# Performance work log

Hardware: AMD Instinct MI355X
Metric: run time of the kernel (lower is better)

The kernel has to match this reference:

```python
import jax, jax.numpy as jnp
import numpy as np

D0, D1, D2, D3 = 128, 256, 512, 256
B, L = 64, 1024


def _glorot(key, shape):
    fan_in = shape[0]
    return jax.random.normal(key, shape, dtype=jnp.float32) / np.sqrt(fan_in)


def setup_inputs() -> dict:
    key = jax.random.key(0)
    ks = jax.random.split(key, 16)
    return {
        "hid_r": jax.random.normal(ks[0], (B, L, D3), dtype=jnp.float32),
        "in_mask": jnp.ones((B, L), dtype=jnp.float32),
        "init_in": jnp.zeros((B, 1, D0), dtype=jnp.float32),
        "h0": jnp.zeros((1, B, D2), dtype=jnp.float32),
        "c0": jnp.zeros((1, B, D2), dtype=jnp.float32),
        # lin_1: D0 -> D1 (Linear + ReLU)
        "W1": _glorot(ks[1], (D0, D1)), "b1": jnp.zeros((D1,), jnp.float32),
        # LSTM: input D1, hidden D2, gates order i,f,g,o (PyTorch)
        "Wih": _glorot(ks[2], (D1, 4 * D2)), "Whh": _glorot(ks[3], (D2, 4 * D2)),
        "bih": jnp.zeros((4 * D2,), jnp.float32), "bhh": jnp.zeros((4 * D2,), jnp.float32),
        # lin_2: D2 -> D3
        "W2": _glorot(ks[4], (D2, D3)), "b2": jnp.zeros((D3,), jnp.float32),
        # attention projections q,k,v (D3 -> D3)
        "Wq": _glorot(ks[5], (D3, D3)), "bq": jnp.zeros((D3,), jnp.float32),
        "Wk": _glorot(ks[6], (D3, D3)), "bk": jnp.zeros((D3,), jnp.float32),
        "Wv": _glorot(ks[7], (D3, D3)), "bv": jnp.zeros((D3,), jnp.float32),
        # lin_3: D3 -> D0
        "W3": _glorot(ks[8], (D3, D0)), "b3": jnp.zeros((D0,), jnp.float32),
    }


def reference(hid_r, in_mask, init_in, h0, c0, W1, b1, Wih, Whh, bih, bhh,
              W2, b2, Wq, bq, Wk, bk, Wv, bv, W3, b3):
    length = hid_r.shape[1]
    scale = 1.0 / np.sqrt(D3).astype(np.float32)
    # k/v projections of the (fixed) encoder memory, hoisted out of the loop
    k = hid_r @ Wk + bk            # [B, L, D3]
    v = hid_r @ Wv + bv            # [B, L, D3]
    mask_bias = jnp.where(in_mask == 0, -1e9, 0.0)  # [B, L]

    def step(carry, _):
        h, c, x = carry            # h,c: [B,D2], x: [B,D0]
        a = jax.nn.relu(x @ W1 + b1)                       # lin_1
        gates = a @ Wih + bih + h @ Whh + bhh              # [B, 4*D2]
        i_g, f_g, g_g, o_g = jnp.split(gates, 4, axis=-1)
        c = jax.nn.sigmoid(f_g) * c + jax.nn.sigmoid(i_g) * jnp.tanh(g_g)
        h = jax.nn.sigmoid(o_g) * jnp.tanh(c)
        dx = jax.nn.relu(h @ W2 + b2)                      # lin_2 -> [B,D3]
        q = dx @ Wq + bq                                   # [B, D3]
        scores = jnp.einsum('bd,bld->bl', q, k) * scale + mask_bias
        attn = jax.nn.softmax(scores, axis=-1)             # [B, L]
        ctx = jnp.einsum('bl,bld->bd', attn, v)            # [B, D3]
        y = jax.nn.relu(ctx @ W3 + b3)                     # lin_3 -> [B,D0]
        return (h, c, y), (y, attn)

    carry0 = (h0[0], c0[0], init_in[:, 0, :])
    _, (ys, attns) = jax.lax.scan(step, carry0, None, length=length)
    outputs = jnp.transpose(ys, (1, 0, 2)) * in_mask[:, :, None]  # mask_it
    attention_weights = jnp.transpose(attns, (1, 0, 2))           # [B, L, L]
    return outputs, attention_weights
```

## Files before the change

### kernel.cpp

```cpp
#include <hip/hip_runtime.h>

typedef unsigned short u16;
typedef unsigned int u32;
typedef __attribute__((ext_vector_type(8))) short bf16x8;
typedef __attribute__((ext_vector_type(8))) unsigned short u16x8;
typedef __attribute__((ext_vector_type(4))) unsigned short u16x4;
typedef __attribute__((ext_vector_type(4))) float f32x4;

#define DI static __device__ __forceinline__

constexpr size_t OFF_WKQ  = 0;
constexpr size_t OFF_WVW  = OFF_WKQ  + 256*256*4;
constexpr size_t OFF_WB   = OFF_WVW  + 256*128*4;
constexpr size_t OFF_BYV  = OFF_WB   + 256*4;
constexpr size_t OFF_BG   = OFF_BYV  + 128*4;
constexpr size_t OFF_W2T  = OFF_BG   + 2048*4;
constexpr size_t OFF_W1F  = OFF_W2T  + 256*512*2;
constexpr size_t OFF_WIHF = OFF_W1F  + 16*4*64*8*2;
constexpr size_t OFF_WHHF = OFF_WIHF + 128*8*64*8*2;
constexpr size_t OFF_KT   = OFF_WHHF + 128*16*64*8*2;
constexpr size_t OFF_VW   = OFF_KT   + (size_t)64*1024*256*2;
constexpr size_t OFF_S0   = OFF_VW   + (size_t)64*1024*128*2;
constexpr size_t OFF_CB   = OFF_S0   + 65536*4;
constexpr size_t OFF_HF   = OFF_CB   + 64*512*4;
constexpr size_t OFF_HFR  = OFF_HF   + 64*512*4;
constexpr size_t OFF_SC   = OFF_HFR  + 2*16*4*64*8*2;
constexpr size_t OFF_PART = OFF_SC   + 2*64*1024*4;

DI float bf2f(u16 u){ unsigned int v = ((unsigned int)u) << 16; return __uint_as_float(v); }
DI u16 f2bf(float f){ unsigned int u = __float_as_uint(f); unsigned int r = (u + 0x7FFFu + ((u>>16)&1u)) >> 16; return (u16)r; }
DI float sigm(float x){ return 1.f/(1.f + __expf(-x)); }
DI float tanh_(float x){ return 1.f - 2.f/(__expf(2.f*x) + 1.f); }

DI int fragIdx(int m, int k){ return (((k>>5)*4 + (m>>4))*64 + ((m&15) | (((k>>3)&3)<<4)))*8 + (k&7); }

__global__ __launch_bounds__(256) void kPrep(char* ws,
    const float* W1, const float* Wih, const float* Whh, const float* W2,
    const float* Wq, const float* bq, const float* Wk, const float* bk,
    const float* Wv, const float* bv, const float* W3, const float* b3,
    const float* bih, const float* bhh, const float* c0, const float* h0)
{
  const int wg = blockIdx.x, tid = threadIdx.x;
  if (wg < 64) {
    float* Wkq = (float*)(ws + OFF_WKQ);
    for (int rr = 0; rr < 4; ++rr) {
      const int e = wg*4 + rr;
      float acc = 0.f;
      for (int d = 0; d < 256; ++d) acc = fmaf(Wk[e*256+d], Wq[tid*256+d], acc);
      Wkq[e*256 + tid] = acc * 0.0625f;
    }
  } else if (wg < 96) {
    float* Wvw = (float*)(ws + OFF_WVW);
    if (tid < 128) {
      for (int rr = 0; rr < 8; ++rr) {
        const int e = (wg-64)*8 + rr;
        float acc = 0.f;
        for (int d = 0; d < 256; ++d) acc = fmaf(Wv[e*256+d], W3[d*128+tid], acc);
        Wvw[e*128 + tid] = acc;
      }
    }
  } else if (wg == 96) {
    float* wb = (float*)(ws + OFF_WB);
    float acc = 0.f;
    for (int d = 0; d < 256; ++d) acc = fmaf(Wk[tid*256+d], bq[d], acc);
    wb[tid] = acc * 0.0625f;
    if (tid < 128) {
      float* byv = (float*)(ws + OFF_BYV);
      float a2 = b3[tid];
      for (int d = 0; d < 256; ++d) a2 = fmaf(bv[d], W3[d*128+tid], a2);
      byv[tid] = a2;
    }
  } else if (wg == 97) {
    float* bg = (float*)(ws + OFF_BG);
    for (int j = tid; j < 2048; j += 256) bg[j] = bih[j] + bhh[j];
  } else if (wg < 106) {
    u16* W2T = (u16*)(ws + OFF_W2T);
    const int n0 = (wg - 98)*32;
    for (int nn = 0; nn < 32; ++nn) {
      const int n = n0 + nn;
      for (int k = tid; k < 512; k += 256) W2T[n*512 + k] = f2bf(W2[k*256 + n]);
    }
  } else if (wg < 122) {
    u16* W1f = (u16*)(ws + OFF_W1F);
    const int nt2 = wg - 106;
    for (int idx = tid; idx < 4*512; idx += 256) {
      const int kt2 = idx >> 9, rem = idx & 511, lane = rem >> 3, i = rem & 7;
      const int k = kt2*32 + (lane>>4)*8 + i, n = nt2*16 + (lane&15);
      W1f[((nt2*4+kt2)*64+lane)*8+i] = f2bf(W1[k*256+n]);
    }
  } else if (wg < 250) {
    u16* Wihf = (u16*)(ws + OFF_WIHF);
    const int nt = wg - 122;
    for (int idx = tid; idx < 8*512; idx += 256) {
      const int kt = idx >> 9, rem = idx & 511, lane = rem >> 3, i = rem & 7;
      const int k = kt*32 + (lane>>4)*8 + i, r = lane & 15;
      const int gcol = (r>>2)*512 + nt*4 + (r&3);
      Wihf[((nt*8+kt)*64+lane)*8+i] = f2bf(Wih[k*2048 + gcol]);
    }
  } else if (wg < 378) {
    u16* Whhf = (u16*)(ws + OFF_WHHF);
    const int nt = wg - 250;
    for (int idx = tid; idx < 16*512; idx += 256) {
      const int kt = idx >> 9, rem = idx & 511, lane = rem >> 3, i = rem & 7;
      const int k = kt*32 + (lane>>4)*8 + i, r = lane & 15;
      const int gcol = (r>>2)*512 + nt*4 + (r&3);
      Whhf[((nt*16+kt)*64+lane)*8+i] = f2bf(Whh[k*2048 + gcol]);
    }
  } else if (wg < 410) {
    float* cb = (float*)(ws + OFF_CB);
    u16* hfr0 = (u16*)(ws + OFF_HFR);
    const int base = (wg - 378)*1024;
    for (int ii = tid; ii < 1024; ii += 256) {
      const int idx = base + ii, b = idx >> 9, j = idx & 511;
      cb[idx] = c0[idx];
      hfr0[fragIdx(b, j)] = f2bf(h0[idx]);
    }
  }
}

__global__ __launch_bounds__(256) void kKTVW(char* __restrict__ ws, const float* __restrict__ hid_r,
                                             const float* __restrict__ in_mask)
{
  const int wg = blockIdx.x, tid = threadIdx.x;
  __shared__ float lh[256*36];
  const float* Wkq = (const float*)(ws + OFF_WKQ);
  const float* Wvw = (const float*)(ws + OFF_WVW);
  const float* wb  = (const float*)(ws + OFF_WB);
  u16* kt = (u16*)(ws + OFF_KT);
  u16* vw = (u16*)(ws + OFF_VW);
  float* s0 = (float*)(ws + OFF_S0);
  const size_t r0 = (size_t)wg * 32;
  for (int idx = tid; idx < 32*256; idx += 256) {
    const int e = idx & 255, r = idx >> 8;
    lh[e*36 + r] = hid_r[(r0 + r)*256 + e];
  }
  __syncthreads();
  float acc[32];
  #pragma unroll
  for (int r = 0; r < 32; ++r) acc[r] = 0.f;
  for (int e = 0; e < 256; ++e) {
    const float wv = Wkq[e*256 + tid];
    #pragma unroll
    for (int r4 = 0; r4 < 8; ++r4) {
      const float4 l4 = *(const float4*)&lh[e*36 + r4*4];
      acc[r4*4+0] = fmaf(l4.x, wv, acc[r4*4+0]);
      acc[r4*4+1] = fmaf(l4.y, wv, acc[r4*4+1]);
      acc[r4*4+2] = fmaf(l4.z, wv, acc[r4*4+2]);
      acc[r4*4+3] = fmaf(l4.w, wv, acc[r4*4+3]);
    }
  }
  for (int r = 0; r < 32; ++r) kt[(r0 + r)*256 + tid] = f2bf(acc[r]);
  if (tid < 128) {
    #pragma unroll
    for (int r = 0; r < 32; ++r) acc[r] = 0.f;
    for (int e = 0; e < 256; ++e) {
      const float wv = Wvw[e*128 + tid];
      #pragma unroll
      for (int r4 = 0; r4 < 8; ++r4) {
        const float4 l4 = *(const float4*)&lh[e*36 + r4*4];
        acc[r4*4+0] = fmaf(l4.x, wv, acc[r4*4+0]);
        acc[r4*4+1] = fmaf(l4.y, wv, acc[r4*4+1]);
        acc[r4*4+2] = fmaf(l4.z, wv, acc[r4*4+2]);
        acc[r4*4+3] = fmaf(l4.w, wv, acc[r4*4+3]);
      }
    }
    for (int r = 0; r < 32; ++r) vw[(r0 + r)*128 + tid] = f2bf(acc[r]);
  } else if (tid < 160) {
    const int r = tid - 128;
    float a3 = 0.f;
    for (int e = 0; e < 256; ++e) a3 = fmaf(lh[e*36 + r], wb[e], a3);
    s0[r0 + r] = a3 + (in_mask[r0 + r] == 0.f ? -1e9f : 0.f);
  }
}

__global__ __launch_bounds__(1024) void kA(char* __restrict__ ws, const float* __restrict__ init_in,
                                           const float* __restrict__ in_mask, const float* __restrict__ b1,
                                           float* __restrict__ dout, int s)
{
  const int wg = blockIdx.x, tid = threadIdx.x;
  const float* part = (const float*)(ws + OFF_PART) + (size_t)((s+1)&1)*(64*8*130);
  const float* byv = (const float*)(ws + OFF_BYV);

  if (wg >= 64) {
    if (s == 0) return;
    const int b = wg - 64, t = s - 1;
    const float* scp = (const float*)(ws + OFF_SC) + (size_t)((s+1)&1)*(64*1024);
    float pm[8], pS[8], m = -1e30f;
    #pragma unroll
    for (int c = 0; c < 8; ++c) { pm[c] = part[(b*8+c)*130]; pS[c] = part[(b*8+c)*130+1]; m = fmaxf(m, pm[c]); }
    float Sv = 0.f;
    #pragma unroll
    for (int c = 0; c < 8; ++c) Sv += pS[c] * __expf(pm[c]-m);
    const float inv = 1.f / Sv;
    float* attn = dout + (size_t)64*1024*128;
    __builtin_nontemporal_store(__expf(scp[b*1024 + tid] - m) * inv,
                                &attn[((size_t)b*1024 + t)*1024 + tid]);
    if (tid < 128) {
      float a2 = 0.f;
      #pragma unroll
      for (int c = 0; c < 8; ++c) a2 += __expf(pm[c]-m) * part[(b*8+c)*130+2+tid];
      const float y = fmaxf(a2*inv + byv[tid], 0.f);
      __builtin_nontemporal_store(y * in_mask[b*1024 + t],
                                  &dout[((size_t)b*1024 + t)*128 + tid]);
    }
    return;
  }

  __shared__ union {
    u16 yfrag[16*64*8];
    struct { float gmerge[8*64*4]; float gtile[64*32]; } s3;
  } shmU;
  __shared__ union {
    u16 afrag[32*64*8];
    float lfac[64*8];
  } shmV;

  if (s == 0) {
    for (int idx = tid; idx < 64*128; idx += 1024) {
      const int b = idx >> 7, d0 = idx & 127;
      shmU.yfrag[fragIdx(b, d0)] = f2bf(init_in[b*128 + d0]);
    }
  } else {
    if (tid < 64) {
      const int b = tid;
      float pm[8], m = -1e30f;
      #pragma unroll
      for (int c = 0; c < 8; ++c) { pm[c] = part[(b*8+c)*130]; m = fmaxf(m, pm[c]); }
      float Sv = 0.f, pf[8];
      #pragma unroll
      for (int c = 0; c < 8; ++c) { pf[c] = __expf(pm[c]-m); Sv += part[(b*8+c)*130+1]*pf[c]; }
      const float inv = 1.f/Sv;
      #pragma unroll
      for (int c = 0; c < 8; ++c) shmV.lfac[b*8+c] = pf[c]*inv;
    }
    __syncthreads();
    for (int idx = tid; idx < 64*128; idx += 1024) {
      const int b = idx >> 7, d0 = idx & 127;
      float a2 = byv[d0];
      #pragma unroll
      for (int c = 0; c < 8; ++c) a2 += shmV.lfac[b*8+c]*part[(b*8+c)*130+2+d0];
      shmU.yfrag[fragIdx(b, d0)] = f2bf(fmaxf(a2, 0.f));
    }
  }
  __syncthreads();
  const int w = tid >> 6, lane = tid & 63;
  {
    const u16* W1f = (const u16*)(ws + OFF_W1F);
    const int mt = w & 3, nb0 = w >> 2;
    for (int k = 0; k < 4; ++k) {
      const int nt2 = nb0 + k*4;
      f32x4 acc = {0.f,0.f,0.f,0.f};
      #pragma unroll
      for (int kt2 = 0; kt2 < 4; ++kt2) {
        bf16x8 av = *(const bf16x8*)&shmU.yfrag[((kt2*4+mt)*64+lane)*8];
        bf16x8 bv = *(const bf16x8*)&W1f[((nt2*4+kt2)*64+lane)*8];
        acc = __builtin_amdgcn_mfma_f32_16x16x32_bf16(av, bv, acc, 0, 0, 0);
      }
      const int col = nt2*16 + (lane&15);
      const float bb = b1[col];
      #pragma unroll
      for (int i = 0; i < 4; ++i) {
        const int b = mt*16 + (lane>>4)*4 + i;
        shmV.afrag[fragIdx(b, col)] = f2bf(fmaxf(acc[i] + bb, 0.f));
      }
    }
  }
  __syncthreads();
  {
    const u16* Wihf = (const u16*)(ws + OFF_WIHF);
    const u16* Whhf = (const u16*)(ws + OFF_WHHF);
    const u16* hfr = (const u16*)(ws + OFF_HFR) + (size_t)(s & 1)*(16*4*64*8);
    const int mt = w & 3, ntile = (w>>2) & 1, khalf = w >> 3;
    const int nt = wg*2 + ntile;
    f32x4 acc = {0.f,0.f,0.f,0.f};
    if (khalf == 0) {
      for (int kt = 0; kt < 8; ++kt) {
        bf16x8 av = *(const bf16x8*)&shmV.afrag[((kt*4+mt)*64+lane)*8];
        bf16x8 bv = *(const bf16x8*)&Wihf[((nt*8+kt)*64+lane)*8];
        acc = __builtin_amdgcn_mfma_f32_16x16x32_bf16(av, bv, acc, 0, 0, 0);
      }
      for (int kt = 0; kt < 4; ++kt) {
        bf16x8 av = *(const bf16x8*)&hfr[((kt*4+mt)*64+lane)*8];
        bf16x8 bv = *(const bf16x8*)&Whhf[((nt*16+kt)*64+lane)*8];
        acc = __builtin_amdgcn_mfma_f32_16x16x32_bf16(av, bv, acc, 0, 0, 0);
      }
    } else {
      for (int kt = 4; kt < 16; ++kt) {
        bf16x8 av = *(const bf16x8*)&hfr[((kt*4+mt)*64+lane)*8];
        bf16x8 bv = *(const bf16x8*)&Whhf[((nt*16+kt)*64+lane)*8];
        acc = __builtin_amdgcn_mfma_f32_16x16x32_bf16(av, bv, acc, 0, 0, 0);
      }
      #pragma unroll
      for (int i = 0; i < 4; ++i) shmU.s3.gmerge[((ntile*4+mt)*64+lane)*4+i] = acc[i];
    }
    __syncthreads();
    if (khalf == 0) {
      const float* bg = (const float*)(ws + OFF_BG);
      const int r = lane & 15;
      const float bb = bg[(r>>2)*512 + nt*4 + (r&3)];
      #pragma unroll
      for (int i = 0; i < 4; ++i) {
        const int b = mt*16 + (lane>>4)*4 + i;
        shmU.s3.gtile[b*32 + ntile*16 + r] = acc[i] + shmU.s3.gmerge[((ntile*4+mt)*64+lane)*4+i] + bb;
      }
    }
  }
  __syncthreads();
  if (tid < 256) {
    const int b = tid >> 2, jj2 = tid & 3;
    float* cb = (float*)(ws + OFF_CB);
    float* hf = (float*)(ws + OFF_HF);
    u16* hfw = (u16*)(ws + OFF_HFR) + (size_t)((s & 1) ^ 1)*(16*4*64*8);
    float hv[2];
    #pragma unroll
    for (int t2 = 0; t2 < 2; ++t2) {
      const int jj = jj2*2 + t2;
      const int j = wg*8 + jj;
      const int cb32 = b*32 + (jj>>2)*16 + (jj&3);
      const float ig = shmU.s3.gtile[cb32 + 0];
      const float fg = shmU.s3.gtile[cb32 + 4];
      const float gg = shmU.s3.gtile[cb32 + 8];
      const float og = shmU.s3.gtile[cb32 + 12];
      const float cold = cb[b*512 + j];
      const float cnew = sigm(fg)*cold + sigm(ig)*tanh_(gg);
      hv[t2] = sigm(og)*tanh_(cnew);
      cb[b*512 + j] = cnew;
    }
    const int j0 = wg*8 + jj2*2;
    *(float2*)&hf[b*512 + j0] = make_float2(hv[0], hv[1]);
    const u32 pw = (u32)f2bf(hv[0]) | ((u32)f2bf(hv[1]) << 16);
    *(u32*)&hfw[fragIdx(b, j0)] = pw;
  }
}

__global__ __launch_bounds__(512, 4) void kB(char* __restrict__ ws, const float* __restrict__ b2, int s)
{
  const int wg = blockIdx.x, tid = threadIdx.x;
  const int b = wg >> 3, ch = wg & 7;
  const int hl = tid & 31, unit = tid >> 5;
  __shared__ union { float red[256*33]; float mrg[16*132]; } U;
  __shared__ float dxl[256];

  const u16* kt = (const u16*)(ws + OFF_KT);
  const u16* vw = (const u16*)(ws + OFF_VW);
  const float* s0 = (const float*)(ws + OFF_S0);
  float* partc = (float*)(ws + OFF_PART) + (size_t)(s&1)*(64*8*130);
  float* scc   = (float*)(ws + OFF_SC)   + (size_t)(s&1)*(64*1024);

  u16x8 kvr[8]; u16x4 vvr[8]; float s0r[8];
  #pragma unroll
  for (int i = 0; i < 8; ++i) {
    const int l = ch*128 + i*16 + unit;
    const size_t row = (size_t)b*1024 + l;
    kvr[i] = *(const u16x8*)(kt + row*256 + hl*8);
    vvr[i] = *(const u16x4*)(vw + row*128 + hl*4);
    s0r[i] = s0[row];
  }

  {
    const float* hb = (const float*)(ws + OFF_HF) + b*512;
    const u16* W2T = (const u16*)(ws + OFF_W2T);
    float hreg[16];
    #pragma unroll
    for (int i = 0; i < 4; ++i) {
      const float4 h4 = *(const float4*)(hb + hl*16 + i*4);
      hreg[i*4+0] = h4.x; hreg[i*4+1] = h4.y; hreg[i*4+2] = h4.z; hreg[i*4+3] = h4.w;
    }
    #pragma unroll
    for (int j = 0; j < 16; ++j) {
      const int n = unit*16 + j;
      const u16x8 w0 = *(const u16x8*)(W2T + n*512 + hl*16);
      const u16x8 w1 = *(const u16x8*)(W2T + n*512 + hl*16 + 8);
      float acc = 0.f;
      #pragma unroll
      for (int i2 = 0; i2 < 8; ++i2) acc = fmaf(hreg[i2], bf2f(w0[i2]), acc);
      #pragma unroll
      for (int i2 = 0; i2 < 8; ++i2) acc = fmaf(hreg[8+i2], bf2f(w1[i2]), acc);
      U.red[n*33 + hl] = acc;
    }
  }
  __syncthreads();
  if (tid < 256) {
    float acc = 0.f;
    #pragma unroll
    for (int l = 0; l < 32; ++l) acc += U.red[tid*33 + l];
    dxl[tid] = fmaxf(acc + b2[tid], 0.f);
  }
  __syncthreads();

  float dxv[8];
  {
    const float4 d0 = *(const float4*)&dxl[hl*8];
    const float4 d1 = *(const float4*)&dxl[hl*8+4];
    dxv[0]=d0.x; dxv[1]=d0.y; dxv[2]=d0.z; dxv[3]=d0.w;
    dxv[4]=d1.x; dxv[5]=d1.y; dxv[6]=d1.z; dxv[7]=d1.w;
  }
  float sums[8];
  #pragma unroll
  for (int i = 0; i < 8; ++i) {
    float sum = 0.f;
    #pragma unroll
    for (int j2 = 0; j2 < 8; ++j2) sum = fmaf(bf2f(kvr[i][j2]), dxv[j2], sum);
    #pragma unroll
    for (int d = 1; d < 32; d <<= 1) sum += __shfl_xor(sum, d, 64);
    sums[i] = sum + s0r[i];
  }
  float keep = 0.f;
  #pragma unroll
  for (int i = 0; i < 8; ++i) if (hl == i) keep = sums[i];
  float m = sums[0];
  #pragma unroll
  for (int i = 1; i < 8; ++i) m = fmaxf(m, sums[i]);
  float S = 0.f, cx0 = 0.f, cx1 = 0.f, cx2 = 0.f, cx3 = 0.f;
  #pragma unroll
  for (int i = 0; i < 8; ++i) {
    const float e2 = __expf(sums[i] - m);
    S += e2;
    cx0 = fmaf(e2, bf2f(vvr[i][0]), cx0);
    cx1 = fmaf(e2, bf2f(vvr[i][1]), cx1);
    cx2 = fmaf(e2, bf2f(vvr[i][2]), cx2);
    cx3 = fmaf(e2, bf2f(vvr[i][3]), cx3);
  }
  if (hl < 8) scc[b*1024 + ch*128 + hl*16 + unit] = keep;
  U.mrg[unit*132 + 4 + hl*4 + 0] = cx0;
  U.mrg[unit*132 + 4 + hl*4 + 1] = cx1;
  U.mrg[unit*132 + 4 + hl*4 + 2] = cx2;
  U.mrg[unit*132 + 4 + hl*4 + 3] = cx3;
  if (hl == 0) { U.mrg[unit*132] = m; U.mrg[unit*132+1] = S; }
  __syncthreads();
  if (tid < 128) {
    float mg = -1e30f;
    for (int u = 0; u < 16; ++u) mg = fmaxf(mg, U.mrg[u*132]);
    float Sg = 0.f, cx = 0.f;
    for (int u = 0; u < 16; ++u) {
      const float f = __expf(U.mrg[u*132] - mg);
      Sg = fmaf(U.mrg[u*132+1], f, Sg);
      cx = fmaf(f, U.mrg[u*132 + 4 + tid], cx);
    }
    partc[(b*8+ch)*130 + 2 + tid] = cx;
    if (tid == 0) { partc[(b*8+ch)*130] = mg; partc[(b*8+ch)*130+1] = Sg; }
  }
}

__global__ __launch_bounds__(1024) void kWLast(char* __restrict__ ws, const float* __restrict__ in_mask,
                                               float* __restrict__ dout)
{
  const int b = blockIdx.x, tid = threadIdx.x;
  const float* part = (const float*)(ws + OFF_PART) + (size_t)(1023&1)*(64*8*130);
  const float* sc   = (const float*)(ws + OFF_SC)   + (size_t)(1023&1)*(64*1024);
  float pm[8], pS[8], m = -1e30f;
  #pragma unroll
  for (int c = 0; c < 8; ++c) { pm[c] = part[(b*8+c)*130]; pS[c] = part[(b*8+c)*130+1]; m = fmaxf(m, pm[c]); }
  float Sv = 0.f;
  #pragma unroll
  for (int c = 0; c < 8; ++c) Sv += pS[c] * __expf(pm[c]-m);
  const float inv = 1.f / Sv;
  float* attn = dout + (size_t)64*1024*128;
  __builtin_nontemporal_store(__expf(sc[b*1024 + tid] - m) * inv,
                              &attn[((size_t)b*1024 + 1023)*1024 + tid]);
  if (tid < 128) {
    const float* byv = (const float*)(ws + OFF_BYV);
    float a2 = 0.f;
    #pragma unroll
    for (int c = 0; c < 8; ++c) a2 += __expf(pm[c]-m) * part[(b*8+c)*130+2+tid];
    const float y = fmaxf(a2*inv + byv[tid], 0.f);
    __builtin_nontemporal_store(y * in_mask[b*1024 + 1023],
                                &dout[((size_t)b*1024 + 1023)*128 + tid]);
  }
}

extern "C" void kernel_launch(void* const* d_in, const int* in_sizes, int n_in,
                              void* d_out, int out_size, void* d_ws, size_t ws_size,
                              hipStream_t stream)
{
  (void)in_sizes; (void)n_in; (void)out_size; (void)ws_size;
  const float* hid_r  = (const float*)d_in[0];
  const float* in_mask= (const float*)d_in[1];
  const float* init_in= (const float*)d_in[2];
  const float* h0     = (const float*)d_in[3];
  const float* c0     = (const float*)d_in[4];
  const float* W1     = (const float*)d_in[5];
  const float* b1     = (const float*)d_in[6];
  const float* Wih    = (const float*)d_in[7];
  const float* Whh    = (const float*)d_in[8];
  const float* bih    = (const float*)d_in[9];
  const float* bhh    = (const float*)d_in[10];
  const float* W2     = (const float*)d_in[11];
  const float* b2     = (const float*)d_in[12];
  const float* Wq     = (const float*)d_in[13];
  const float* bq     = (const float*)d_in[14];
  const float* Wk     = (const float*)d_in[15];
  const float* bk     = (const float*)d_in[16];
  const float* Wv     = (const float*)d_in[17];
  const float* bv     = (const float*)d_in[18];
  const float* W3     = (const float*)d_in[19];
  const float* b3     = (const float*)d_in[20];
  char* ws = (char*)d_ws;
  float* out = (float*)d_out;

  hipLaunchKernelGGL(kPrep, dim3(410), dim3(256), 0, stream, ws,
                     W1, Wih, Whh, W2, Wq, bq, Wk, bk, Wv, bv, W3, b3, bih, bhh, c0, h0);
  hipLaunchKernelGGL(kKTVW, dim3(2048), dim3(256), 0, stream, ws, hid_r, in_mask);
  for (int s = 0; s < 1024; ++s) {
    hipLaunchKernelGGL(kA, dim3(128), dim3(1024), 0, stream, ws, init_in, in_mask, b1, out, s);
    hipLaunchKernelGGL(kB, dim3(512), dim3(512), 0, stream, ws, b2, s);
  }
  hipLaunchKernelGGL(kWLast, dim3(64), dim3(1024), 0, stream, ws, in_mask, out);
}
```

Measured before the change: 29.23 ms.

## Fuse per-step LSTM and attention kernels with in-kernel flag synchronization

Merges the two per-timestep launches into a single kernel of 512 workgroups. Workgroups 0-63 compute the LSTM gates, then spin on global epoch flags until every gate group has published h. Each then computes dx for its batch row and signals the attention workgroups through a per-batch flag. This halves the launch count and the kernel-boundary drains per step, and lets attention work for other batches start without a full grid barrier. The cost is spin-waiting that assumes all workgroups are co-resident, which risks deadlock or contention, plus a redundant dx matvec per batch in the gate workgroups.

```diff
diff --git a/kernel.cpp b/kernel.cpp
--- a/kernel.cpp
+++ b/kernel.cpp
@@ -2,6 +2,7 @@
 
 typedef unsigned short u16;
 typedef unsigned int u32;
+typedef unsigned long long u64;
 typedef __attribute__((ext_vector_type(8))) short bf16x8;
 typedef __attribute__((ext_vector_type(8))) unsigned short u16x8;
 typedef __attribute__((ext_vector_type(4))) unsigned short u16x4;
@@ -26,11 +27,20 @@
 constexpr size_t OFF_HFR  = OFF_HF   + 64*512*4;
 constexpr size_t OFF_SC   = OFF_HFR  + 2*16*4*64*8*2;
 constexpr size_t OFF_PART = OFF_SC   + 2*64*1024*4;
+constexpr size_t OFF_DXG  = OFF_PART + 2*64*8*130*4;
+constexpr size_t OFF_HFL  = OFF_DXG  + 64*256*4;
+constexpr size_t OFF_DXF  = OFF_HFL  + 64*16*4;
 
 DI float bf2f(u16 u){ unsigned int v = ((unsigned int)u) << 16; return __uint_as_float(v); }
 DI u16 f2bf(float f){ unsigned int u = __float_as_uint(f); unsigned int r = (u + 0x7FFFu + ((u>>16)&1u)) >> 16; return (u16)r; }
 DI float sigm(float x){ return 1.f/(1.f + __expf(-x)); }
 DI float tanh_(float x){ return 1.f - 2.f/(__expf(2.f*x) + 1.f); }
+
+DI float aldf(const float* p){ return __hip_atomic_load(p, __ATOMIC_RELAXED, __HIP_MEMORY_SCOPE_AGENT); }
+DI void  astf(float* p, float v){ __hip_atomic_store(p, v, __ATOMIC_RELAXED, __HIP_MEMORY_SCOPE_AGENT); }
+DI void  astu32(u32* p, u32 v){ __hip_atomic_store(p, v, __ATOMIC_RELAXED, __HIP_MEMORY_SCOPE_AGENT); }
+DI u32   aldu32(const u32* p){ return __hip_atomic_load(p, __ATOMIC_RELAXED, __HIP_MEMORY_SCOPE_AGENT); }
+DI void  astu64(u64* p, u64 v){ __hip_atomic_store(p, v, __ATOMIC_RELAXED, __HIP_MEMORY_SCOPE_AGENT); }
 
 DI int fragIdx(int m, int k){ return (((k>>5)*4 + (m>>4))*64 + ((m&15) | (((k>>3)&3)<<4)))*8 + (k&7); }
 
@@ -73,6 +83,8 @@
   } else if (wg == 97) {
     float* bg = (float*)(ws + OFF_BG);
     for (int j = tid; j < 2048; j += 256) bg[j] = bih[j] + bhh[j];
+    u32* fl = (u32*)(ws + OFF_HFL);
+    for (int j = tid; j < 2048; j += 256) fl[j] = 0u;
   } else if (wg < 106) {
     u16* W2T = (u16*)(ws + OFF_W2T);
     const int n0 = (wg - 98)*32;
@@ -173,18 +185,43 @@
   }
 }
 
-__global__ __launch_bounds__(1024) void kA(char* __restrict__ ws, const float* __restrict__ init_in,
-                                           const float* __restrict__ in_mask, const float* __restrict__ b1,
-                                           float* __restrict__ dout, int s)
+struct ShmGates {
+  union {
+    u16 yfrag[16*64*8];
+    float gtile[64*32];
+    struct { float hstage[512]; float dxred[512]; } dxs;
+  } u;
+  union {
+    u16 afrag[32*64*8];
+    float lfac[64*8];
+  } v;
+};
+struct ShmAttn { float mrg[16*132]; float dxl[256]; };
+union Shm { ShmGates g; ShmAttn a; };
+
+__global__ __launch_bounds__(512, 4) void kStep(char* __restrict__ ws, const float* __restrict__ init_in,
+    const float* __restrict__ in_mask, const float* __restrict__ b1, const float* __restrict__ b2,
+    float* __restrict__ dout, int s)
 {
   const int wg = blockIdx.x, tid = threadIdx.x;
+  __shared__ Shm sh;
+
   const float* part = (const float*)(ws + OFF_PART) + (size_t)((s+1)&1)*(64*8*130);
+  float* partc = (float*)(ws + OFF_PART) + (size_t)(s&1)*(64*8*130);
+  const float* scp = (const float*)(ws + OFF_SC) + (size_t)((s+1)&1)*(64*1024);
+  float* scc = (float*)(ws + OFF_SC) + (size_t)(s&1)*(64*1024);
   const float* byv = (const float*)(ws + OFF_BYV);
-
-  if (wg >= 64) {
-    if (s == 0) return;
-    const int b = wg - 64, t = s - 1;
-    const float* scp = (const float*)(ws + OFF_SC) + (size_t)((s+1)&1)*(64*1024);
+  float* HF = (float*)(ws + OFF_HF);
+  float* dxg = (float*)(ws + OFF_DXG);
+  u32* hfl = (u32*)(ws + OFF_HFL);
+  u32* dxf = (u32*)(ws + OFF_DXF);
+  const u32 epoch = (u32)s + 1u;
+
+  int b, ch;
+  if (wg < 64) { b = wg; ch = 7; }
+  else { const int a = wg - 64; b = a / 7; ch = a % 7; }
+
+  if (s > 0 && tid < 256) {
     float pm[8], pS[8], m = -1e30f;
     #pragma unroll
     for (int c = 0; c < 8; ++c) { pm[c] = part[(b*8+c)*130]; pS[c] = part[(b*8+c)*130+1]; m = fmaxf(m, pm[c]); }
@@ -192,253 +229,242 @@
     #pragma unroll
     for (int c = 0; c < 8; ++c) Sv += pS[c] * __expf(pm[c]-m);
     const float inv = 1.f / Sv;
-    float* attn = dout + (size_t)64*1024*128;
-    __builtin_nontemporal_store(__expf(scp[b*1024 + tid] - m) * inv,
-                                &attn[((size_t)b*1024 + t)*1024 + tid]);
+    const int t = s - 1;
     if (tid < 128) {
+      const int l = ch*128 + tid;
+      float* attn = dout + (size_t)64*1024*128;
+      __builtin_nontemporal_store(__expf(scp[b*1024 + l] - m) * inv,
+                                  &attn[((size_t)b*1024 + t)*1024 + l]);
+    } else if (ch == 0) {
+      const int d0 = tid - 128;
       float a2 = 0.f;
       #pragma unroll
-      for (int c = 0; c < 8; ++c) a2 += __expf(pm[c]-m) * part[(b*8+c)*130+2+tid];
-      const float y = fmaxf(a2*inv + byv[tid], 0.f);
+      for (int c = 0; c < 8; ++c) a2 += __expf(pm[c]-m) * part[(b*8+c)*130+2+d0];
+      const float y = fmaxf(a2*inv + byv[d0], 0.f);
       __builtin_nontemporal_store(y * in_mask[b*1024 + t],
-                                  &dout[((size_t)b*1024 + t)*128 + tid]);
-    }
-    return;
-  }
-
-  __shared__ union {
-    u16 yfrag[16*64*8];
-    struct { float gmerge[8*64*4]; float gtile[64*32]; } s3;
-  } shmU;
-  __shared__ union {
-    u16 afrag[32*64*8];
-    float lfac[64*8];
-  } shmV;
-
-  if (s == 0) {
-    for (int idx = tid; idx < 64*128; idx += 1024) {
-      const int b = idx >> 7, d0 = idx & 127;
-      shmU.yfrag[fragIdx(b, d0)] = f2bf(init_in[b*128 + d0]);
-    }
-  } else {
-    if (tid < 64) {
-      const int b = tid;
-      float pm[8], m = -1e30f;
-      #pragma unroll
-      for (int c = 0; c < 8; ++c) { pm[c] = part[(b*8+c)*130]; m = fmaxf(m, pm[c]); }
-      float Sv = 0.f, pf[8];
-      #pragma unroll
-      for (int c = 0; c < 8; ++c) { pf[c] = __expf(pm[c]-m); Sv += part[(b*8+c)*130+1]*pf[c]; }
-      const float inv = 1.f/Sv;
-      #pragma unroll
-      for (int c = 0; c < 8; ++c) shmV.lfac[b*8+c] = pf[c]*inv;
-    }
-    __syncthreads();
-    for (int idx = tid; idx < 64*128; idx += 1024) {
-      const int b = idx >> 7, d0 = idx & 127;
-      float a2 = byv[d0];
-      #pragma unroll
-      for (int c = 0; c < 8; ++c) a2 += shmV.lfac[b*8+c]*part[(b*8+c)*130+2+d0];
-      shmU.yfrag[fragIdx(b, d0)] = f2bf(fmaxf(a2, 0.f));
-    }
-  }
-  __syncthreads();
-  const int w = tid >> 6, lane = tid & 63;
-  {
-    const u16* W1f = (const u16*)(ws + OFF_W1F);
-    const int mt = w & 3, nb0 = w >> 2;
-    for (int k = 0; k < 4; ++k) {
-      const int nt2 = nb0 + k*4;
+                                  &dout[((size_t)b*1024 + t)*128 + d0]);
+    }
+  }
+
+  const int hl = tid & 31, unit = tid >> 5;
+
+  if (wg < 64) {
+    if (s == 0) {
+      for (int idx = tid; idx < 64*128; idx += 512) {
+        const int bb = idx >> 7, d0 = idx & 127;
+        sh.g.u.yfrag[fragIdx(bb, d0)] = f2bf(init_in[bb*128 + d0]);
+      }
+    } else {
+      if (tid < 64) {
+        const int bb = tid;
+        float pm[8], m = -1e30f;
+        #pragma unroll
+        for (int c = 0; c < 8; ++c) { pm[c] = part[(bb*8+c)*130]; m = fmaxf(m, pm[c]); }
+        float Sv = 0.f, pf[8];
+        #pragma unroll
+        for (int c = 0; c < 8; ++c) { pf[c] = __expf(pm[c]-m); Sv += part[(bb*8+c)*130+1]*pf[c]; }
+        const float inv = 1.f/Sv;
+        #pragma unroll
+        for (int c = 0; c < 8; ++c) sh.g.v.lfac[bb*8+c] = pf[c]*inv;
+      }
+      __syncthreads();
+      for (int idx = tid; idx < 64*128; idx += 512) {
+        const int bb = idx >> 7, d0 = idx & 127;
+        float a2 = byv[d0];
+        #pragma unroll
+        for (int c = 0; c < 8; ++c) a2 += sh.g.v.lfac[bb*8+c]*part[(bb*8+c)*130+2+d0];
+        sh.g.u.yfrag[fragIdx(bb, d0)] = f2bf(fmaxf(a2, 0.f));
+      }
+    }
+    __syncthreads();
+    const int w = tid >> 6, lane = tid & 63;
+    {
+      const u16* W1f = (const u16*)(ws + OFF_W1F);
+      const int mt = w & 3, nh = w >> 2;
+      for (int k = 0; k < 8; ++k) {
+        const int nt2 = nh*8 + k;
+        f32x4 acc = {0.f,0.f,0.f,0.f};
+        #pragma unroll
+        for (int kt2 = 0; kt2 < 4; ++kt2) {
+          bf16x8 av = *(const bf16x8*)&sh.g.u.yfrag[((kt2*4+mt)*64+lane)*8];
+          bf16x8 bv = *(const bf16x8*)&W1f[((nt2*4+kt2)*64+lane)*8];
+          acc = __builtin_amdgcn_mfma_f32_16x16x32_bf16(av, bv, acc, 0, 0, 0);
+        }
+        const int col = nt2*16 + (lane&15);
+        const float bb2 = b1[col];
+        #pragma unroll
+        for (int i = 0; i < 4; ++i) {
+          const int bb = mt*16 + (lane>>4)*4 + i;
+          sh.g.v.afrag[fragIdx(bb, col)] = f2bf(fmaxf(acc[i] + bb2, 0.f));
+        }
+      }
+    }
+    __syncthreads();
+    {
+      const u16* Wihf = (const u16*)(ws + OFF_WIHF);
+      const u16* Whhf = (const u16*)(ws + OFF_WHHF);
+      const u16* hfr = (const u16*)(ws + OFF_HFR) + (size_t)(s & 1)*(16*4*64*8);
+      const int mt = w & 3, ntile = w >> 2;
+      const int nt = wg*2 + ntile;
       f32x4 acc = {0.f,0.f,0.f,0.f};
-      #pragma unroll
-      for (int kt2 = 0; kt2 < 4; ++kt2) {
-        bf16x8 av = *(const bf16x8*)&shmU.yfrag[((kt2*4+mt)*64+lane)*8];
-        bf16x8 bv = *(const bf16x8*)&W1f[((nt2*4+kt2)*64+lane)*8];
-        acc = __builtin_amdgcn_mfma_f32_16x16x32_bf16(av, bv, acc, 0, 0, 0);
-      }
-      const int col = nt2*16 + (lane&15);
-      const float bb = b1[col];
-      #pragma unroll
-      for (int i = 0; i < 4; ++i) {
-        const int b = mt*16 + (lane>>4)*4 + i;
-        shmV.afrag[fragIdx(b, col)] = f2bf(fmaxf(acc[i] + bb, 0.f));
-      }
-    }
-  }
-  __syncthreads();
-  {
-    const u16* Wihf = (const u16*)(ws + OFF_WIHF);
-    const u16* Whhf = (const u16*)(ws + OFF_WHHF);
-    const u16* hfr = (const u16*)(ws + OFF_HFR) + (size_t)(s & 1)*(16*4*64*8);
-    const int mt = w & 3, ntile = (w>>2) & 1, khalf = w >> 3;
-    const int nt = wg*2 + ntile;
-    f32x4 acc = {0.f,0.f,0.f,0.f};
-    if (khalf == 0) {
       for (int kt = 0; kt < 8; ++kt) {
-        bf16x8 av = *(const bf16x8*)&shmV.afrag[((kt*4+mt)*64+lane)*8];
+        bf16x8 av = *(const bf16x8*)&sh.g.v.afrag[((kt*4+mt)*64+lane)*8];
         bf16x8 bv = *(const bf16x8*)&Wihf[((nt*8+kt)*64+lane)*8];
         acc = __builtin_amdgcn_mfma_f32_16x16x32_bf16(av, bv, acc, 0, 0, 0);
       }
-      for (int kt = 0; kt < 4; ++kt) {
+      for (int kt = 0; kt < 16; ++kt) {
         bf16x8 av = *(const bf16x8*)&hfr[((kt*4+mt)*64+lane)*8];
         bf16x8 bv = *(const bf16x8*)&Whhf[((nt*16+kt)*64+lane)*8];
         acc = __builtin_amdgcn_mfma_f32_16x16x32_bf16(av, bv, acc, 0, 0, 0);
       }
-    } else {
-      for (int kt = 4; kt < 16; ++kt) {
-        bf16x8 av = *(const bf16x8*)&hfr[((kt*4+mt)*64+lane)*8];
-        bf16x8 bv = *(const bf16x8*)&Whhf[((nt*16+kt)*64+lane)*8];
-        acc = __builtin_amdgcn_mfma_f32_16x16x32_bf16(av, bv, acc, 0, 0, 0);
-      }
-      #pragma unroll
-      for (int i = 0; i < 4; ++i) shmU.s3.gmerge[((ntile*4+mt)*64+lane)*4+i] = acc[i];
-    }
-    __syncthreads();
-    if (khalf == 0) {
+      __syncthreads();
       const float* bg = (const float*)(ws + OFF_BG);
       const int r = lane & 15;
-      const float bb = bg[(r>>2)*512 + nt*4 + (r&3)];
+      const float bb2 = bg[(r>>2)*512 + nt*4 + (r&3)];
       #pragma unroll
       for (int i = 0; i < 4; ++i) {
-        const int b = mt*16 + (lane>>4)*4 + i;
-        shmU.s3.gtile[b*32 + ntile*16 + r] = acc[i] + shmU.s3.gmerge[((ntile*4+mt)*64+lane)*4+i] + bb;
-      }
-    }
-  }
-  __syncthreads();
-  if (tid < 256) {
-    const int b = tid >> 2, jj2 = tid & 3;
-    float* cb = (float*)(ws + OFF_CB);
-    float* hf = (float*)(ws + OFF_HF);
-    u16* hfw = (u16*)(ws + OFF_HFR) + (size_t)((s & 1) ^ 1)*(16*4*64*8);
-    float hv[2];
-    #pragma unroll
-    for (int t2 = 0; t2 < 2; ++t2) {
-      const int jj = jj2*2 + t2;
-      const int j = wg*8 + jj;
-      const int cb32 = b*32 + (jj>>2)*16 + (jj&3);
-      const float ig = shmU.s3.gtile[cb32 + 0];
-      const float fg = shmU.s3.gtile[cb32 + 4];
-      const float gg = shmU.s3.gtile[cb32 + 8];
-      const float og = shmU.s3.gtile[cb32 + 12];
-      const float cold = cb[b*512 + j];
-      const float cnew = sigm(fg)*cold + sigm(ig)*tanh_(gg);
-      hv[t2] = sigm(og)*tanh_(cnew);
-      cb[b*512 + j] = cnew;
-    }
-    const int j0 = wg*8 + jj2*2;
-    *(float2*)&hf[b*512 + j0] = make_float2(hv[0], hv[1]);
-    const u32 pw = (u32)f2bf(hv[0]) | ((u32)f2bf(hv[1]) << 16);
-    *(u32*)&hfw[fragIdx(b, j0)] = pw;
-  }
-}
-
-__global__ __launch_bounds__(512, 4) void kB(char* __restrict__ ws, const float* __restrict__ b2, int s)
-{
-  const int wg = blockIdx.x, tid = threadIdx.x;
-  const int b = wg >> 3, ch = wg & 7;
-  const int hl = tid & 31, unit = tid >> 5;
-  __shared__ union { float red[256*33]; float mrg[16*132]; } U;
-  __shared__ float dxl[256];
-
-  const u16* kt = (const u16*)(ws + OFF_KT);
-  const u16* vw = (const u16*)(ws + OFF_VW);
-  const float* s0 = (const float*)(ws + OFF_S0);
-  float* partc = (float*)(ws + OFF_PART) + (size_t)(s&1)*(64*8*130);
-  float* scc   = (float*)(ws + OFF_SC)   + (size_t)(s&1)*(64*1024);
-
-  u16x8 kvr[8]; u16x4 vvr[8]; float s0r[8];
-  #pragma unroll
-  for (int i = 0; i < 8; ++i) {
-    const int l = ch*128 + i*16 + unit;
-    const size_t row = (size_t)b*1024 + l;
-    kvr[i] = *(const u16x8*)(kt + row*256 + hl*8);
-    vvr[i] = *(const u16x4*)(vw + row*128 + hl*4);
-    s0r[i] = s0[row];
+        const int bb = mt*16 + (lane>>4)*4 + i;
+        sh.g.u.gtile[bb*32 + ntile*16 + r] = acc[i] + bb2;
+      }
+    }
+    __syncthreads();
+    if (tid < 256) {
+      const int bb = tid >> 2, jj2 = tid & 3;
+      float* cb = (float*)(ws + OFF_CB);
+      u16* hfw = (u16*)(ws + OFF_HFR) + (size_t)((s & 1) ^ 1)*(16*4*64*8);
+      float hv[2];
+      #pragma unroll
+      for (int t2 = 0; t2 < 2; ++t2) {
+        const int jj = jj2*2 + t2;
+        const int j = wg*8 + jj;
+        const int cb32 = bb*32 + (jj>>2)*16 + (jj&3);
+        const float ig = sh.g.u.gtile[cb32 + 0];
+        const float fg = sh.g.u.gtile[cb32 + 4];
+        const float gg = sh.g.u.gtile[cb32 + 8];
+        const float og = sh.g.u.gtile[cb32 + 12];
+        const float cold = cb[bb*512 + j];
+        const float cnew = sigm(fg)*cold + sigm(ig)*tanh_(gg);
+        hv[t2] = sigm(og)*tanh_(cnew);
+        cb[bb*512 + j] = cnew;
+      }
+      const int j0 = wg*8 + jj2*2;
+      union { float f[2]; u64 u; } pk; pk.f[0] = hv[0]; pk.f[1] = hv[1];
+      astu64((u64*)&HF[bb*512 + j0], pk.u);
+      const u32 pw = (u32)f2bf(hv[0]) | ((u32)f2bf(hv[1]) << 16);
+      *(u32*)&hfw[fragIdx(bb, j0)] = pw;
+    }
+    __syncthreads();
+    if (tid == 0) astu32(&hfl[wg*16], epoch);
+    if (tid < 64) {
+      for (;;) {
+        const u32 f = aldu32(&hfl[tid*16]);
+        if (__all(f >= epoch)) break;
+        __builtin_amdgcn_s_sleep(1);
+      }
+    }
+    __syncthreads();
+    sh.g.u.dxs.hstage[tid] = aldf(&HF[b*512 + tid]);
+    __syncthreads();
+    float dxval = 0.f;
+    {
+      const u16* W2T = (const u16*)(ws + OFF_W2T);
+      const int n = tid >> 1, kh = tid & 1;
+      float acc = 0.f;
+      for (int kk = 0; kk < 32; ++kk) {
+        const int k = kh*256 + kk*8;
+        const float4 h4a = *(const float4*)&sh.g.u.dxs.hstage[k];
+        const float4 h4b = *(const float4*)&sh.g.u.dxs.hstage[k+4];
+        const u16x8 wv = *(const u16x8*)(W2T + n*512 + k);
+        acc = fmaf(h4a.x, bf2f(wv[0]), acc); acc = fmaf(h4a.y, bf2f(wv[1]), acc);
+        acc = fmaf(h4a.z, bf2f(wv[2]), acc); acc = fmaf(h4a.w, bf2f(wv[3]), acc);
+        acc = fmaf(h4b.x, bf2f(wv[4]), acc); acc = fmaf(h4b.y, bf2f(wv[5]), acc);
+        acc = fmaf(h4b.z, bf2f(wv[6]), acc); acc = fmaf(h4b.w, bf2f(wv[7]), acc);
+      }
+      sh.g.u.dxs.dxred[tid] = acc;
+      __syncthreads();
+      if (tid < 256) dxval = fmaxf(sh.g.u.dxs.dxred[2*tid] + sh.g.u.dxs.dxred[2*tid+1] + b2[tid], 0.f);
+    }
+    __syncthreads();
+    if (tid < 256) {
+      sh.a.dxl[tid] = dxval;
+      astf(&dxg[b*256 + tid], dxval);
+    }
+    __syncthreads();
+    if (tid == 0) astu32(&dxf[b*16], epoch);
+  } else {
+    if (tid == 0) {
+      while (aldu32(&dxf[b*16]) < epoch) __builtin_amdgcn_s_sleep(2);
+    }
+    __syncthreads();
+    if (tid < 256) sh.a.dxl[tid] = aldf(&dxg[b*256 + tid]);
+    __syncthreads();
   }
 
   {
-    const float* hb = (const float*)(ws + OFF_HF) + b*512;
-    const u16* W2T = (const u16*)(ws + OFF_W2T);
-    float hreg[16];
-    #pragma unroll
-    for (int i = 0; i < 4; ++i) {
-      const float4 h4 = *(const float4*)(hb + hl*16 + i*4);
-      hreg[i*4+0] = h4.x; hreg[i*4+1] = h4.y; hreg[i*4+2] = h4.z; hreg[i*4+3] = h4.w;
-    }
-    #pragma unroll
-    for (int j = 0; j < 16; ++j) {
-      const int n = unit*16 + j;
-      const u16x8 w0 = *(const u16x8*)(W2T + n*512 + hl*16);
-      const u16x8 w1 = *(const u16x8*)(W2T + n*512 + hl*16 + 8);
-      float acc = 0.f;
+    const u16* kt = (const u16*)(ws + OFF_KT);
+    const u16* vw = (const u16*)(ws + OFF_VW);
+    const float* s0 = (const float*)(ws + OFF_S0);
+    u16x8 kvr[8]; u16x4 vvr[8]; float s0r[8];
+    #pragma unroll
+    for (int i = 0; i < 8; ++i) {
+      const int l = ch*128 + i*16 + unit;
+      const size_t row = (size_t)b*1024 + l;
+      kvr[i] = *(const u16x8*)(kt + row*256 + hl*8);
+      vvr[i] = *(const u16x4*)(vw + row*128 + hl*4);
+      s0r[i] = s0[row];
+    }
+    float dxv[8];
+    {
+      const float4 d0 = *(const float4*)&sh.a.dxl[hl*8];
+      const float4 d1 = *(const float4*)&sh.a.dxl[hl*8+4];
+      dxv[0]=d0.x; dxv[1]=d0.y; dxv[2]=d0.z; dxv[3]=d0.w;
+      dxv[4]=d1.x; dxv[5]=d1.y; dxv[6]=d1.z; dxv[7]=d1.w;
+    }
+    float sums[8];
+    #pragma unroll
+    for (int i = 0; i < 8; ++i) {
+      float sum = 0.f;
       #pragma unroll
-      for (int i2 = 0; i2 < 8; ++i2) acc = fmaf(hreg[i2], bf2f(w0[i2]), acc);
+      for (int j2 = 0; j2 < 8; ++j2) sum = fmaf(bf2f(kvr[i][j2]), dxv[j2], sum);
       #pragma unroll
-      for (int i2 = 0; i2 < 8; ++i2) acc = fmaf(hreg[8+i2], bf2f(w1[i2]), acc);
-      U.red[n*33 + hl] = acc;
-    }
-  }
-  __syncthreads();
-  if (tid < 256) {
-    float acc = 0.f;
-    #pragma unroll
-    for (int l = 0; l < 32; ++l) acc += U.red[tid*33 + l];
-    dxl[tid] = fmaxf(acc + b2[tid], 0.f);
-  }
-  __syncthreads();
-
-  float dxv[8];
-  {
-    const float4 d0 = *(const float4*)&dxl[hl*8];
-    const float4 d1 = *(const float4*)&dxl[hl*8+4];
-    dxv[0]=d0.x; dxv[1]=d0.y; dxv[2]=d0.z; dxv[3]=d0.w;
-    dxv[4]=d1.x; dxv[5]=d1.y; dxv[6]=d1.z; dxv[7]=d1.w;
-  }
-  float sums[8];
-  #pragma unroll
-  for (int i = 0; i < 8; ++i) {
-    float sum = 0.f;
-    #pragma unroll
-    for (int j2 = 0; j2 < 8; ++j2) sum = fmaf(bf2f(kvr[i][j2]), dxv[j2], sum);
-    #pragma unroll
-    for (int d = 1; d < 32; d <<= 1) sum += __shfl_xor(sum, d, 64);
-    sums[i] = sum + s0r[i];
-  }
-  float keep = 0.f;
-  #pragma unroll
-  for (int i = 0; i < 8; ++i) if (hl == i) keep = sums[i];
-  float m = sums[0];
-  #pragma unroll
-  for (int i = 1; i < 8; ++i) m = fmaxf(m, sums[i]);
-  float S = 0.f, cx0 = 0.f, cx1 = 0.f, cx2 = 0.f, cx3 = 0.f;
-  #pragma unroll
-  for (int i = 0; i < 8; ++i) {
-    const float e2 = __expf(sums[i] - m);
-    S += e2;
-    cx0 = fmaf(e2, bf2f(vvr[i][0]), cx0);
-    cx1 = fmaf(e2, bf2f(vvr[i][1]), cx1);
-    cx2 = fmaf(e2, bf2f(vvr[i][2]), cx2);
-    cx3 = fmaf(e2, bf2f(vvr[i][3]), cx3);
-  }
-  if (hl < 8) scc[b*1024 + ch*128 + hl*16 + unit] = keep;
-  U.mrg[unit*132 + 4 + hl*4 + 0] = cx0;
-  U.mrg[unit*132 + 4 + hl*4 + 1] = cx1;
-  U.mrg[unit*132 + 4 + hl*4 + 2] = cx2;
-  U.mrg[unit*132 + 4 + hl*4 + 3] = cx3;
-  if (hl == 0) { U.mrg[unit*132] = m; U.mrg[unit*132+1] = S; }
-  __syncthreads();
-  if (tid < 128) {
-    float mg = -1e30f;
-    for (int u = 0; u < 16; ++u) mg = fmaxf(mg, U.mrg[u*132]);
-    float Sg = 0.f, cx = 0.f;
-    for (int u = 0; u < 16; ++u) {
-      const float f = __expf(U.mrg[u*132] - mg);
-      Sg = fmaf(U.mrg[u*132+1], f, Sg);
-      cx = fmaf(f, U.mrg[u*132 + 4 + tid], cx);
-    }
-    partc[(b*8+ch)*130 + 2 + tid] = cx;
-    if (tid == 0) { partc[(b*8+ch)*130] = mg; partc[(b*8+ch)*130+1] = Sg; }
+      for (int d = 1; d < 32; d <<= 1) sum += __shfl_xor(sum, d, 64);
+      sums[i] = sum + s0r[i];
+    }
+    float keep = 0.f;
+    #pragma unroll
+    for (int i = 0; i < 8; ++i) if (hl == i) keep = sums[i];
+    float m = sums[0];
+    #pragma unroll
+    for (int i = 1; i < 8; ++i) m = fmaxf(m, sums[i]);
+    float S = 0.f, cx0 = 0.f, cx1 = 0.f, cx2 = 0.f, cx3 = 0.f;
+    #pragma unroll
+    for (int i = 0; i < 8; ++i) {
+      const float e2 = __expf(sums[i] - m);
+      S += e2;
+      cx0 = fmaf(e2, bf2f(vvr[i][0]), cx0);
+      cx1 = fmaf(e2, bf2f(vvr[i][1]), cx1);
+      cx2 = fmaf(e2, bf2f(vvr[i][2]), cx2);
+      cx3 = fmaf(e2, bf2f(vvr[i][3]), cx3);
+    }
+    if (hl < 8) scc[b*1024 + ch*128 + hl*16 + unit] = keep;
+    sh.a.mrg[unit*132 + 4 + hl*4 + 0] = cx0;
+    sh.a.mrg[unit*132 + 4 + hl*4 + 1] = cx1;
+    sh.a.mrg[unit*132 + 4 + hl*4 + 2] = cx2;
+    sh.a.mrg[unit*132 + 4 + hl*4 + 3] = cx3;
+    if (hl == 0) { sh.a.mrg[unit*132] = m; sh.a.mrg[unit*132+1] = S; }
+    __syncthreads();
+    if (tid < 128) {
+      float mg = -1e30f;
+      for (int u = 0; u < 16; ++u) mg = fmaxf(mg, sh.a.mrg[u*132]);
+      float Sg = 0.f, cx = 0.f;
+      for (int u = 0; u < 16; ++u) {
+        const float f = __expf(sh.a.mrg[u*132] - mg);
+        Sg = fmaf(sh.a.mrg[u*132+1], f, Sg);
+        cx = fmaf(f, sh.a.mrg[u*132 + 4 + tid], cx);
+      }
+      partc[(b*8+ch)*130 + 2 + tid] = cx;
+      if (tid == 0) { partc[(b*8+ch)*130] = mg; partc[(b*8+ch)*130+1] = Sg; }
+    }
   }
 }
 
@@ -502,8 +528,7 @@
                      W1, Wih, Whh, W2, Wq, bq, Wk, bk, Wv, bv, W3, b3, bih, bhh, c0, h0);
   hipLaunchKernelGGL(kKTVW, dim3(2048), dim3(256), 0, stream, ws, hid_r, in_mask);
   for (int s = 0; s < 1024; ++s) {
-    hipLaunchKernelGGL(kA, dim3(128), dim3(1024), 0, stream, ws, init_in, in_mask, b1, out, s);
-    hipLaunchKernelGGL(kB, dim3(512), dim3(512), 0, stream, ws, b2, s);
+    hipLaunchKernelGGL(kStep, dim3(512), dim3(512), 0, stream, ws, init_in, in_mask, b1, b2, out, s);
   }
   hipLaunchKernelGGL(kWLast, dim3(64), dim3(1024), 0, stream, ws, in_mask, out);
 }
```

Measured after the change: 36.46 ms. 1.25x slower.
